# Performance work log

Measured on AMD Instinct MI355X. Metric: run time of the kernel, lower is better.

## Reference

```python
import jax, jax.numpy as jnp
import numpy as np

N, E = 50000, 1600000
IN_DIM, OUT_DIM = 256, 256


def setup_inputs() -> dict:
    key = jax.random.key(0)
    ks = jax.random.split(key, 9)
    def xavier(k, shape):
        fan_in, fan_out = shape[1], shape[0]
        a = jnp.sqrt(6.0 / (fan_in + fan_out))
        return jax.random.uniform(k, shape, jnp.float32, -a, a)
    return {
        "x": jax.random.normal(ks[0], (N, IN_DIM), jnp.float32),
        "edge_index": jax.random.randint(ks[1], (2, E), 0, N, jnp.int64 if jax.config.jax_enable_x64 else jnp.int32),
        "edge_attr": jax.random.uniform(ks[2], (E,), jnp.float32),
        # GCNConv linear (no bias inside lin; bias added after aggregation)
        "W_gcn": xavier(ks[3], (OUT_DIM, IN_DIM)),
        "b_gcn": jnp.zeros((OUT_DIM,), jnp.float32),
        # MLP: Linear(in+out -> out), tanh, Linear(out -> out), tanh
        "W1": xavier(ks[4], (OUT_DIM, IN_DIM + OUT_DIM)),
        "b1": jnp.zeros((OUT_DIM,), jnp.float32),
        "W2": xavier(ks[5], (OUT_DIM, OUT_DIM)),
        "b2": jnp.zeros((OUT_DIM,), jnp.float32),
    }


def gcn_conv(x, edge_index, W, b):
    n = x.shape[0]
    # add self loops
    loops = jnp.arange(n, dtype=edge_index.dtype)
    row = jnp.concatenate([edge_index[0], loops])  # source
    col = jnp.concatenate([edge_index[1], loops])  # target
    # symmetric normalization with edge_weight = 1
    deg = jax.ops.segment_sum(jnp.ones_like(col, dtype=x.dtype), col, num_segments=n)
    dinv = jnp.where(deg > 0, jax.lax.rsqrt(deg), 0.0)
    norm = dinv[row] * dinv[col]  # [E+N]
    xw = x @ W.T  # [N, out_dim]
    msgs = xw[row] * norm[:, None]  # gather + scale
    out = jax.ops.segment_sum(msgs, col, num_segments=n)  # scatter-add
    return out + b


def reference(x, edge_index, edge_attr, W_gcn, b_gcn, W1, b1, W2, b2):
    # edge_attr is accepted but unused by the original module's routing
    x1 = jnp.tanh(gcn_conv(x, edge_index, W_gcn, b_gcn))
    h = jnp.concatenate([x, x1], axis=1)  # [N, in+out]
    h = jnp.tanh(h @ W1.T + b1)
    return jnp.tanh(h @ W2.T + b2)
```

## Files before the change

### kernel.cpp

```cpp
#include <hip/hip_runtime.h>
#include <stdint.h>

typedef __attribute__((ext_vector_type(8))) short bf16x8_t;
typedef __attribute__((ext_vector_type(4))) float f32x4_t;

#define GLOAD_LDS16(gp, lp) __builtin_amdgcn_global_load_lds( \
    (__attribute__((address_space(1))) void*)(void*)(gp),      \
    (__attribute__((address_space(3))) void*)(lp), 16, 0, 0)

#define CSR_STRIDE 96

__device__ __forceinline__ float bf2f(unsigned short u) {
  union { unsigned int i; float f; } c; c.i = ((unsigned int)u) << 16; return c.f;
}
__device__ __forceinline__ unsigned short f2bf(float f) {
  unsigned int x = __float_as_uint(f);
  unsigned int r = (x + 0x7fffu + ((x >> 16) & 1u)) >> 16;
  return (unsigned short)r;
}
__device__ __forceinline__ float fast_tanh(float x) {
  const float cx = fminf(fmaxf(x, -15.f), 15.f);
  const float e  = __expf(2.f * cx);
  return __fdividef(e - 1.f, e + 1.f);
}

__global__ void prep_kernel(const float* __restrict__ x, unsigned short* __restrict__ xh,
                            const float* __restrict__ Wg, const float* __restrict__ W1,
                            const float* __restrict__ W2, unsigned short* __restrict__ Wg_b,
                            unsigned short* __restrict__ W1_b, unsigned short* __restrict__ W2_b,
                            int* __restrict__ cursor, unsigned short* __restrict__ xws,
                            int n, int total) {
  const int gid = blockIdx.x * blockDim.x + threadIdx.x;
  const int i = gid * 4;
  if (i < total) {
    float4 v = *(const float4*)(x + i);
    int row = i >> 8, col = i & 255;
    ushort4 o;
    o.x = f2bf(v.x); o.y = f2bf(v.y); o.z = f2bf(v.z); o.w = f2bf(v.w);
    *(ushort4*)(xh + (size_t)row * 512 + col) = o;
  }
  if (gid < n) cursor[gid] = 0;
  if (gid < 256) xws[((size_t)(gid >> 5) * (n + 1) + n) * 32 + (gid & 31)] = 0;
  if (gid < 65536) {
    const float* src; unsigned short* dst; int off;
    if (i < 65536)              { src = Wg; dst = Wg_b; off = i; }
    else if (i < 65536 + 131072){ src = W1; dst = W1_b; off = i - 65536; }
    else                        { src = W2; dst = W2_b; off = i - (65536 + 131072); }
    float4 v = *(const float4*)(src + off);
    ushort4 o;
    o.x = f2bf(v.x); o.y = f2bf(v.y); o.z = f2bf(v.z); o.w = f2bf(v.w);
    *(ushort4*)(dst + off) = o;
  }
}

__global__ void fill_kernel(const int* __restrict__ esrc, const int* __restrict__ edst,
                            int* __restrict__ cursor, unsigned short* __restrict__ csr16, int E) {
  int i = blockIdx.x * blockDim.x + threadIdx.x;
  if (i < E) {
    int d = edst[i];
    int pos = atomicAdd(&cursor[d], 1);
    if (pos < CSR_STRIDE) csr16[(size_t)d * CSR_STRIDE + pos] = (unsigned short)esrc[i];
  }
}

__global__ __launch_bounds__(256)
void agg_kernel(const unsigned short* __restrict__ xws, const unsigned short* __restrict__ csr16,
                const int* __restrict__ cursor, const float* __restrict__ bias,
                unsigned short* __restrict__ xh, int n) {
  const int tid   = threadIdx.x;
  const int wid   = tid >> 6;
  const int lane  = tid & 63;
  const int slice = blockIdx.x & 7;
  const int node  = (blockIdx.x >> 3) * 4 + wid;
  if (node >= n) return;
  const int g   = lane >> 3;
  const int gl4 = (lane & 7) * 4;
  const unsigned short* sbase = xws + (size_t)slice * (n + 1) * 32 + gl4;
  const int ZROW = n;

  float a0 = 0.f, a1 = 0.f, a2 = 0.f, a3 = 0.f;
  const int cnt = cursor[node];
  const unsigned short* crow = csr16 + (size_t)node * CSR_STRIDE;
  for (int base = 0; base <= cnt; base += 64) {
    const int il = base + lane;
    int pv = (int)crow[il];
    pv = (il == cnt) ? node : pv;
    const int rem = cnt - base;
#pragma unroll
    for (int b = 0; b < 8; ++b) {
      const int idx = b * 8 + g;
      const int sv  = __builtin_amdgcn_ds_bpermute(idx << 2, pv);
      const int src = (idx <= rem) ? sv : ZROW;
      const ushort4 v = *(const ushort4*)(sbase + ((unsigned)src << 5));
      a0 += bf2f(v.x); a1 += bf2f(v.y); a2 += bf2f(v.z); a3 += bf2f(v.w);
    }
  }
#pragma unroll
  for (int mask = 8; mask < 64; mask <<= 1) {
    a0 += __shfl_xor(a0, mask);
    a1 += __shfl_xor(a1, mask);
    a2 += __shfl_xor(a2, mask);
    a3 += __shfl_xor(a3, mask);
  }
  if (lane < 8) {
    const float di = rsqrtf((float)(cnt + 1));
    const int c0 = slice * 32 + gl4;
    ushort4 o;
    o.x = f2bf(fast_tanh(a0 * di + bias[c0 + 0]));
    o.y = f2bf(fast_tanh(a1 * di + bias[c0 + 1]));
    o.z = f2bf(fast_tanh(a2 * di + bias[c0 + 2]));
    o.w = f2bf(fast_tanh(a3 * di + bias[c0 + 3]));
    *(ushort4*)(xh + (size_t)node * 512 + 256 + c0) = o;
  }
}

__global__ __launch_bounds__(256, 2)
void gemm1_kernel(const unsigned short* __restrict__ A, int lda,
                  const unsigned short* __restrict__ B,
                  const int* __restrict__ degc,
                  unsigned short* __restrict__ Cp, int M, int K) {
  __shared__ __align__(16) unsigned short As[128 * 64];
  __shared__ __align__(16) unsigned short Bs[128 * 64];
  const int tid  = threadIdx.x;
  const int lane = tid & 63;
  const int wid  = tid >> 6;
  const int wm = wid & 1, wn = wid >> 1;
  const int tileM = blockIdx.x * 128;
  const int tileN = blockIdx.y * 128;

  const int rowInCh = lane >> 3;
  const int slot    = lane & 7;
  const int srcOff  = ((slot ^ rowInCh) * 8);

  f32x4_t acc[4][4];
#pragma unroll
  for (int m = 0; m < 4; ++m)
#pragma unroll
    for (int n = 0; n < 4; ++n) acc[m][n] = (f32x4_t){0.f, 0.f, 0.f, 0.f};

  for (int kt = 0; kt < K; kt += 64) {
#pragma unroll
    for (int cc = 0; cc < 4; ++cc) {
      const int c = wid * 4 + cc;
      const int r = c * 8 + rowInCh;
      const int rA = min(tileM + r, M - 1);
      GLOAD_LDS16(A + (size_t)rA * lda + (kt + srcOff), As + c * 512 + lane * 8);
      GLOAD_LDS16(B + (size_t)(tileN + r) * K + (kt + srcOff), Bs + c * 512 + lane * 8);
    }
    __syncthreads();
#pragma unroll
    for (int ks = 0; ks < 2; ++ks) {
      bf16x8_t af[4], bfr[4];
      const int ksl = ks * 4 + (lane >> 4);
#pragma unroll
      for (int m = 0; m < 4; ++m) {
        const int ra = wm * 64 + m * 16 + (lane & 15);
        af[m]  = *(const bf16x8_t*)(As + ra * 64 + ((ksl ^ (ra & 7)) * 8));
        const int rb = wn * 64 + m * 16 + (lane & 15);
        bfr[m] = *(const bf16x8_t*)(Bs + rb * 64 + ((ksl ^ (rb & 7)) * 8));
      }
#pragma unroll
      for (int m = 0; m < 4; ++m)
#pragma unroll
        for (int n = 0; n < 4; ++n)
          acc[m][n] = __builtin_amdgcn_mfma_f32_16x16x32_bf16(af[m], bfr[n], acc[m][n], 0, 0, 0);
    }
    __syncthreads();
  }

  const int colBase = tileN + wn * 64 + (lane & 15);
  const int rowBase = tileM + wm * 64 + ((lane >> 4) << 2);
#pragma unroll
  for (int m = 0; m < 4; ++m) {
    const int gr0 = rowBase + m * 16;
#pragma unroll
    for (int r = 0; r < 4; ++r) {
      const int gr = gr0 + r;
      if (gr < M) {
        const float rs = rsqrtf((float)(degc[gr] + 1));
#pragma unroll
        for (int n = 0; n < 4; ++n) {
          const int gc = colBase + n * 16;
          Cp[((size_t)(gc >> 5) * (M + 1) + gr) * 32 + (gc & 31)] = f2bf(acc[m][n][r] * rs);
        }
      }
    }
  }
}

__global__ __launch_bounds__(256, 2)
void gemm23_kernel(const unsigned short* __restrict__ A,
                   const unsigned short* __restrict__ W1b,
                   const float* __restrict__ b1,
                   const unsigned short* __restrict__ W2b,
                   const float* __restrict__ b2,
                   float* __restrict__ out, int M) {
  __shared__ __align__(16) unsigned short As[128 * 64];
  __shared__ __align__(16) unsigned short Bs[128 * 64];
  __shared__ __align__(16) unsigned short Hs[128 * 128];
  const int tid  = threadIdx.x;
  const int lane = tid & 63;
  const int wid  = tid >> 6;
  const int wm = wid & 1, wn = wid >> 1;
  const int tileM = blockIdx.x * 128;

  const int rowInCh = lane >> 3;
  const int slot    = lane & 7;
  const int srcOff  = ((slot ^ rowInCh) * 8);

  f32x4_t acc3[4][8];
#pragma unroll
  for (int m = 0; m < 4; ++m)
#pragma unroll
    for (int n = 0; n < 8; ++n) acc3[m][n] = (f32x4_t){0.f, 0.f, 0.f, 0.f};

  const int colB = wn * 64 + (lane & 15);
  const int rowB = wm * 64 + ((lane >> 4) << 2);

#pragma unroll
  for (int half = 0; half < 2; ++half) {
    f32x4_t acc2[4][4];
#pragma unroll
    for (int m = 0; m < 4; ++m)
#pragma unroll
      for (int n = 0; n < 4; ++n) acc2[m][n] = (f32x4_t){0.f, 0.f, 0.f, 0.f};

    for (int kt = 0; kt < 512; kt += 64) {
#pragma unroll
      for (int cc = 0; cc < 4; ++cc) {
        const int c = wid * 4 + cc;
        const int r = c * 8 + rowInCh;
        const int rA = min(tileM + r, M - 1);
        GLOAD_LDS16(A + (size_t)rA * 512 + (kt + srcOff), As + c * 512 + lane * 8);
        GLOAD_LDS16(W1b + (size_t)(half * 128 + r) * 512 + (kt + srcOff), Bs + c * 512 + lane * 8);
      }
      __syncthreads();
#pragma unroll
      for (int ks = 0; ks < 2; ++ks) {
        bf16x8_t af[4], bfr[4];
        const int ksl = ks * 4 + (lane >> 4);
#pragma unroll
        for (int m = 0; m < 4; ++m) {
          const int ra = wm * 64 + m * 16 + (lane & 15);
          af[m]  = *(const bf16x8_t*)(As + ra * 64 + ((ksl ^ (ra & 7)) * 8));
          const int rb = wn * 64 + m * 16 + (lane & 15);
          bfr[m] = *(const bf16x8_t*)(Bs + rb * 64 + ((ksl ^ (rb & 7)) * 8));
        }
#pragma unroll
        for (int m = 0; m < 4; ++m)
#pragma unroll
          for (int n = 0; n < 4; ++n)
            acc2[m][n] = __builtin_amdgcn_mfma_f32_16x16x32_bf16(af[m], bfr[n], acc2[m][n], 0, 0, 0);
      }
      __syncthreads();
    }
#pragma unroll
    for (int n = 0; n < 4; ++n) {
      const int gcl = colB + n * 16;
      const float bv = b1[half * 128 + gcl];
#pragma unroll
      for (int m = 0; m < 4; ++m) {
#pragma unroll
        for (int r = 0; r < 4; ++r) {
          const int row = rowB + m * 16 + r;
          Hs[row * 128 + (gcl ^ ((row & 7) * 8))] = f2bf(fast_tanh(acc2[m][n][r] + bv));
        }
      }
    }
    __syncthreads();
#pragma unroll
    for (int nh = 0; nh < 2; ++nh) {
#pragma unroll
      for (int ks2 = 0; ks2 < 2; ++ks2) {
#pragma unroll
        for (int cc = 0; cc < 4; ++cc) {
          const int c = wid * 4 + cc;
          const int r = c * 8 + rowInCh;
          GLOAD_LDS16(W2b + (size_t)(nh * 128 + r) * 256 + (half * 128 + ks2 * 64 + srcOff),
                      Bs + c * 512 + lane * 8);
        }
        __syncthreads();
#pragma unroll
        for (int ks = 0; ks < 2; ++ks) {
          bf16x8_t af[4], bfr[4];
          const int sl = ks2 * 8 + ks * 4 + (lane >> 4);
          const int ksl = ks * 4 + (lane >> 4);
#pragma unroll
          for (int m = 0; m < 4; ++m) {
            const int ra = wm * 64 + m * 16 + (lane & 15);
            const int slp = (sl & 8) | ((sl & 7) ^ (ra & 7));
            af[m]  = *(const bf16x8_t*)(Hs + ra * 128 + slp * 8);
            const int rb = wn * 64 + m * 16 + (lane & 15);
            bfr[m] = *(const bf16x8_t*)(Bs + rb * 64 + ((ksl ^ (rb & 7)) * 8));
          }
#pragma unroll
          for (int m = 0; m < 4; ++m)
#pragma unroll
            for (int n = 0; n < 4; ++n)
              acc3[m][nh * 4 + n] = __builtin_amdgcn_mfma_f32_16x16x32_bf16(af[m], bfr[n], acc3[m][nh * 4 + n], 0, 0, 0);
        }
        __syncthreads();
      }
    }
  }
#pragma unroll
  for (int nh = 0; nh < 2; ++nh) {
#pragma unroll
    for (int n = 0; n < 4; ++n) {
      const int gc = nh * 128 + colB + n * 16;
      const float bv = b2[gc];
#pragma unroll
      for (int m = 0; m < 4; ++m) {
#pragma unroll
        for (int r = 0; r < 4; ++r) {
          const int gr = tileM + rowB + m * 16 + r;
          if (gr < M) out[(size_t)gr * 256 + gc] = fast_tanh(acc3[m][nh * 4 + n][r] + bv);
        }
      }
    }
  }
}

extern "C" void kernel_launch(void* const* d_in, const int* in_sizes, int n_in,
                              void* d_out, int out_size, void* d_ws, size_t ws_size,
                              hipStream_t stream) {
  const float* x  = (const float*)d_in[0];
  const int*   ei = (const int*)d_in[1];
  const float* Wg = (const float*)d_in[3];
  const float* bg = (const float*)d_in[4];
  const float* W1 = (const float*)d_in[5];
  const float* b1 = (const float*)d_in[6];
  const float* W2 = (const float*)d_in[7];
  const float* b2 = (const float*)d_in[8];
  float* out = (float*)d_out;

  const int N = in_sizes[0] / 256;
  const int E = in_sizes[1] / 2;
  const int* esrc = ei;
  const int* edst = ei + E;

  unsigned short* xh = (unsigned short*)d_out;

  uint8_t* p = (uint8_t*)d_ws;
  auto alloc = [&](size_t bytes) { uint8_t* q = p; p += (bytes + 255) & ~(size_t)255; return q; };
  unsigned short* xws   = (unsigned short*)alloc((size_t)8 * (N + 1) * 32 * 2);
  unsigned short* Wg_b  = (unsigned short*)alloc(256 * 256 * 2);
  unsigned short* W1_b  = (unsigned short*)alloc(256 * 512 * 2);
  unsigned short* W2_b  = (unsigned short*)alloc(256 * 256 * 2);
  int*            cursor= (int*)alloc((size_t)N * 4);
  unsigned short* csr16 = (unsigned short*)alloc(((size_t)N * CSR_STRIDE + 64) * 2);
  (void)ws_size; (void)n_in;

  prep_kernel<<<(N * 256 / 4 + 255) / 256, 256, 0, stream>>>(
      x, xh, Wg, W1, W2, Wg_b, W1_b, W2_b, cursor, xws, N, N * 256);
  fill_kernel<<<(E + 255) / 256, 256, 0, stream>>>(esrc, edst, cursor, csr16, E);

  dim3 g1_grid((N + 127) / 128, 2);
  gemm1_kernel<<<g1_grid, 256, 0, stream>>>(xh, 512, Wg_b, cursor, xws, N, 256);
  agg_kernel<<<8 * ((N + 3) / 4), 256, 0, stream>>>(xws, csr16, cursor, bg, xh, N);
  gemm23_kernel<<<(N + 127) / 128, 256, 0, stream>>>(xh, W1_b, b1, W2_b, b2, out, N);
}
```

Measured before the change: 403.0 us.

## Split fused two-layer MLP GEMM into two separate tiled GEMM launches

Replaces the fused gemm23 kernel, which kept the tanh hidden activation in shared memory and chained both MLP layers per 128-row tile, with a generic templated GEMM launched twice over a 2D grid. The hidden activation now goes through a bf16 workspace buffer in global memory. The aim is more blocks (2x grid), lower shared memory and registers per block, and no serialized second phase. The cost is an extra global write and read of an N×256 bf16 intermediate plus one more launch.

```diff
diff --git a/kernel.cpp b/kernel.cpp
--- a/kernel.cpp
+++ b/kernel.cpp
@@ -188,133 +188,78 @@
   }
 }
 
+template<bool TANH, int OUT_MODE>
 __global__ __launch_bounds__(256, 2)
-void gemm23_kernel(const unsigned short* __restrict__ A,
-                   const unsigned short* __restrict__ W1b,
-                   const float* __restrict__ b1,
-                   const unsigned short* __restrict__ W2b,
-                   const float* __restrict__ b2,
-                   float* __restrict__ out, int M) {
+void gemm_bt_kernel(const unsigned short* __restrict__ A, int lda,
+                    const unsigned short* __restrict__ B,
+                    const float* __restrict__ bias,
+                    void* __restrict__ Cp, int ldc, int M, int K) {
   __shared__ __align__(16) unsigned short As[128 * 64];
   __shared__ __align__(16) unsigned short Bs[128 * 64];
-  __shared__ __align__(16) unsigned short Hs[128 * 128];
   const int tid  = threadIdx.x;
   const int lane = tid & 63;
   const int wid  = tid >> 6;
   const int wm = wid & 1, wn = wid >> 1;
   const int tileM = blockIdx.x * 128;
+  const int tileN = blockIdx.y * 128;
 
   const int rowInCh = lane >> 3;
   const int slot    = lane & 7;
   const int srcOff  = ((slot ^ rowInCh) * 8);
 
-  f32x4_t acc3[4][8];
+  f32x4_t acc[4][4];
 #pragma unroll
   for (int m = 0; m < 4; ++m)
 #pragma unroll
-    for (int n = 0; n < 8; ++n) acc3[m][n] = (f32x4_t){0.f, 0.f, 0.f, 0.f};
-
-  const int colB = wn * 64 + (lane & 15);
-  const int rowB = wm * 64 + ((lane >> 4) << 2);
-
-#pragma unroll
-  for (int half = 0; half < 2; ++half) {
-    f32x4_t acc2[4][4];
-#pragma unroll
-    for (int m = 0; m < 4; ++m)
-#pragma unroll
-      for (int n = 0; n < 4; ++n) acc2[m][n] = (f32x4_t){0.f, 0.f, 0.f, 0.f};
-
-    for (int kt = 0; kt < 512; kt += 64) {
-#pragma unroll
-      for (int cc = 0; cc < 4; ++cc) {
-        const int c = wid * 4 + cc;
-        const int r = c * 8 + rowInCh;
-        const int rA = min(tileM + r, M - 1);
-        GLOAD_LDS16(A + (size_t)rA * 512 + (kt + srcOff), As + c * 512 + lane * 8);
-        GLOAD_LDS16(W1b + (size_t)(half * 128 + r) * 512 + (kt + srcOff), Bs + c * 512 + lane * 8);
+    for (int n = 0; n < 4; ++n) acc[m][n] = (f32x4_t){0.f, 0.f, 0.f, 0.f};
+
+  for (int kt = 0; kt < K; kt += 64) {
+#pragma unroll
+    for (int cc = 0; cc < 4; ++cc) {
+      const int c = wid * 4 + cc;
+      const int r = c * 8 + rowInCh;
+      const int rA = min(tileM + r, M - 1);
+      GLOAD_LDS16(A + (size_t)rA * lda + (kt + srcOff), As + c * 512 + lane * 8);
+      GLOAD_LDS16(B + (size_t)(tileN + r) * K + (kt + srcOff), Bs + c * 512 + lane * 8);
+    }
+    __syncthreads();
+#pragma unroll
+    for (int ks = 0; ks < 2; ++ks) {
+      bf16x8_t af[4], bfr[4];
+      const int ksl = ks * 4 + (lane >> 4);
+#pragma unroll
+      for (int m = 0; m < 4; ++m) {
+        const int ra = wm * 64 + m * 16 + (lane & 15);
+        af[m]  = *(const bf16x8_t*)(As + ra * 64 + ((ksl ^ (ra & 7)) * 8));
+        const int rb = wn * 64 + m * 16 + (lane & 15);
+        bfr[m] = *(const bf16x8_t*)(Bs + rb * 64 + ((ksl ^ (rb & 7)) * 8));
       }
-      __syncthreads();
-#pragma unroll
-      for (int ks = 0; ks < 2; ++ks) {
-        bf16x8_t af[4], bfr[4];
-        const int ksl = ks * 4 + (lane >> 4);
-#pragma unroll
-        for (int m = 0; m < 4; ++m) {
-          const int ra = wm * 64 + m * 16 + (lane & 15);
-          af[m]  = *(const bf16x8_t*)(As + ra * 64 + ((ksl ^ (ra & 7)) * 8));
-          const int rb = wn * 64 + m * 16 + (lane & 15);
-          bfr[m] = *(const bf16x8_t*)(Bs + rb * 64 + ((ksl ^ (rb & 7)) * 8));
-        }
-#pragma unroll
-        for (int m = 0; m < 4; ++m)
-#pragma unroll
-          for (int n = 0; n < 4; ++n)
-            acc2[m][n] = __builtin_amdgcn_mfma_f32_16x16x32_bf16(af[m], bfr[n], acc2[m][n], 0, 0, 0);
-      }
-      __syncthreads();
-    }
-#pragma unroll
-    for (int n = 0; n < 4; ++n) {
-      const int gcl = colB + n * 16;
-      const float bv = b1[half * 128 + gcl];
-#pragma unroll
-      for (int m = 0; m < 4; ++m) {
-#pragma unroll
-        for (int r = 0; r < 4; ++r) {
-          const int row = rowB + m * 16 + r;
-          Hs[row * 128 + (gcl ^ ((row & 7) * 8))] = f2bf(fast_tanh(acc2[m][n][r] + bv));
-        }
-      }
+#pragma unroll
+      for (int m = 0; m < 4; ++m)
+#pragma unroll
+        for (int n = 0; n < 4; ++n)
+          acc[m][n] = __builtin_amdgcn_mfma_f32_16x16x32_bf16(af[m], bfr[n], acc[m][n], 0, 0, 0);
     }
     __syncthreads();
-#pragma unroll
-    for (int nh = 0; nh < 2; ++nh) {
-#pragma unroll
-      for (int ks2 = 0; ks2 < 2; ++ks2) {
-#pragma unroll
-        for (int cc = 0; cc < 4; ++cc) {
-          const int c = wid * 4 + cc;
-          const int r = c * 8 + rowInCh;
-          GLOAD_LDS16(W2b + (size_t)(nh * 128 + r) * 256 + (half * 128 + ks2 * 64 + srcOff),
-                      Bs + c * 512 + lane * 8);
-        }
-        __syncthreads();
-#pragma unroll
-        for (int ks = 0; ks < 2; ++ks) {
-          bf16x8_t af[4], bfr[4];
-          const int sl = ks2 * 8 + ks * 4 + (lane >> 4);
-          const int ksl = ks * 4 + (lane >> 4);
-#pragma unroll
-          for (int m = 0; m < 4; ++m) {
-            const int ra = wm * 64 + m * 16 + (lane & 15);
-            const int slp = (sl & 8) | ((sl & 7) ^ (ra & 7));
-            af[m]  = *(const bf16x8_t*)(Hs + ra * 128 + slp * 8);
-            const int rb = wn * 64 + m * 16 + (lane & 15);
-            bfr[m] = *(const bf16x8_t*)(Bs + rb * 64 + ((ksl ^ (rb & 7)) * 8));
-          }
-#pragma unroll
-          for (int m = 0; m < 4; ++m)
-#pragma unroll
-            for (int n = 0; n < 4; ++n)
-              acc3[m][nh * 4 + n] = __builtin_amdgcn_mfma_f32_16x16x32_bf16(af[m], bfr[n], acc3[m][nh * 4 + n], 0, 0, 0);
-        }
-        __syncthreads();
-      }
-    }
-  }
-#pragma unroll
-  for (int nh = 0; nh < 2; ++nh) {
-#pragma unroll
-    for (int n = 0; n < 4; ++n) {
-      const int gc = nh * 128 + colB + n * 16;
-      const float bv = b2[gc];
-#pragma unroll
-      for (int m = 0; m < 4; ++m) {
-#pragma unroll
-        for (int r = 0; r < 4; ++r) {
-          const int gr = tileM + rowB + m * 16 + r;
-          if (gr < M) out[(size_t)gr * 256 + gc] = fast_tanh(acc3[m][nh * 4 + n][r] + bv);
+  }
+
+  const int colBase = tileN + wn * 64 + (lane & 15);
+  const int rowBase = tileM + wm * 64 + ((lane >> 4) << 2);
+#pragma unroll
+  for (int n = 0; n < 4; ++n) {
+    const int gc = colBase + n * 16;
+    const float bv = bias[gc];
+#pragma unroll
+    for (int m = 0; m < 4; ++m) {
+      const int gr0 = rowBase + m * 16;
+#pragma unroll
+      for (int r = 0; r < 4; ++r) {
+        const int gr = gr0 + r;
+        if (gr < M) {
+          float v = acc[m][n][r] + bv;
+          if (TANH) v = fast_tanh(v);
+          if (OUT_MODE == 0) ((float*)Cp)[(size_t)gr * ldc + gc] = v;
+          else               ((unsigned short*)Cp)[(size_t)gr * ldc + gc] = f2bf(v);
         }
       }
     }
@@ -344,6 +289,7 @@
   uint8_t* p = (uint8_t*)d_ws;
   auto alloc = [&](size_t bytes) { uint8_t* q = p; p += (bytes + 255) & ~(size_t)255; return q; };
   unsigned short* xws   = (unsigned short*)alloc((size_t)8 * (N + 1) * 32 * 2);
+  unsigned short* h2    = (unsigned short*)alloc((size_t)N * 256 * 2);
   unsigned short* Wg_b  = (unsigned short*)alloc(256 * 256 * 2);
   unsigned short* W1_b  = (unsigned short*)alloc(256 * 512 * 2);
   unsigned short* W2_b  = (unsigned short*)alloc(256 * 256 * 2);
@@ -355,8 +301,9 @@
       x, xh, Wg, W1, W2, Wg_b, W1_b, W2_b, cursor, xws, N, N * 256);
   fill_kernel<<<(E + 255) / 256, 256, 0, stream>>>(esrc, edst, cursor, csr16, E);
 
-  dim3 g1_grid((N + 127) / 128, 2);
-  gemm1_kernel<<<g1_grid, 256, 0, stream>>>(xh, 512, Wg_b, cursor, xws, N, 256);
+  dim3 gemm_grid((N + 127) / 128, 2);
+  gemm1_kernel<<<gemm_grid, 256, 0, stream>>>(xh, 512, Wg_b, cursor, xws, N, 256);
   agg_kernel<<<8 * ((N + 3) / 4), 256, 0, stream>>>(xws, csr16, cursor, bg, xh, N);
-  gemm23_kernel<<<(N + 127) / 128, 256, 0, stream>>>(xh, W1_b, b1, W2_b, b2, out, N);
-}
+  gemm_bt_kernel<true, 1><<<gemm_grid, 256, 0, stream>>>(xh, 512, W1_b, b1, h2, 256, N, 512);
+  gemm_bt_kernel<true, 0><<<gemm_grid, 256, 0, stream>>>(h2, 256, W2_b, b2, out, 256, N, 256);
+}
```

After: 351.6 us. 1.15x faster.
